# Optimization experiments

Hardware: AMD Instinct MI355X
Metric: run time of the kernel (lower is better)

Reference implementation:

```python
import jax, jax.numpy as jnp
import numpy as np

MIN_NORM = 1e-15
BALL_EPS = 1e-5  # keep points strictly inside the unit ball (c = 1)


def _artanh(x):
    return jnp.arctanh(jnp.clip(x, -1.0 + BALL_EPS, 1.0 - BALL_EPS))


def expmap0(u):
    # Poincare ball exp map at the origin, c = 1
    n = jnp.clip(jnp.linalg.norm(u, axis=-1, keepdims=True), MIN_NORM)
    return jnp.tanh(n) * u / n


def mobius_matvec(M, x):
    # Mobius matrix-vector product applied to every row of x: [N, D] -> [N, D]
    x_n = jnp.clip(jnp.linalg.norm(x, axis=-1, keepdims=True), MIN_NORM)
    Mx = x @ M.T
    Mx_n = jnp.clip(jnp.linalg.norm(Mx, axis=-1, keepdims=True), MIN_NORM)
    return jnp.tanh(Mx_n / x_n * _artanh(x_n)) * Mx / Mx_n


def pairwise_sqdist(x):
    # sqdist(x_i, x_j) for all pairs via mobius_add(-x_i, x_j); x: [N, D] -> [N, N]
    u = -x[:, None, :]          # [N, 1, D]
    v = x[None, :, :]           # [1, N, D]
    xy = jnp.sum(u * v, axis=-1, keepdims=True)   # [N, N, 1]
    x2 = jnp.sum(u * u, axis=-1, keepdims=True)
    y2 = jnp.sum(v * v, axis=-1, keepdims=True)
    num = (1.0 + 2.0 * xy + y2) * u + (1.0 - x2) * v   # [N, N, D]
    den = jnp.clip(1.0 + 2.0 * xy + x2 * y2, MIN_NORM)
    ma_n = jnp.linalg.norm(num / den, axis=-1)          # [N, N]
    d = 2.0 * _artanh(ma_n)
    return d * d


def setup_inputs() -> dict:
    key = jax.random.key(0)
    k1, k2, k3 = jax.random.split(key, 3)
    N, D, L = 512, 256, 2
    H_euc = jax.random.normal(k1, (N, D), dtype=jnp.float32)
    att_W = jax.random.normal(k2, (L, D, D), dtype=jnp.float32) / np.sqrt(D)
    A = jax.random.randint(k3, (N, N), 0, 2).astype(bool)
    return {"H_euc": H_euc, "att_W": att_W, "A": A}


def reference(H_euc, att_W, A):
    H = expmap0(H_euc)                      # [N, D] on the Poincare ball
    L = att_W.shape[0]
    for l in range(L):
        Wh = mobius_matvec(att_W[l], H)     # one mobius matvec per node (hoisted out of the i,j loop)
        scores = pairwise_sqdist(Wh)        # [N, N] hyperbolic squared distances
        scores = jnp.where(A, scores, -10000.0)
        att = jax.nn.softmax(scores, axis=1)
        att = jnp.where(A, att, 0.0)
        H = att @ H                         # [N, D]
    return H
```

## Files before the change

### kernel.cpp

```cpp
#include <hip/hip_runtime.h>
#include <math.h>

#define NN 512
#define DD 256

__device__ __forceinline__ void wred_sum2(double& a, double& b){
  #pragma unroll
  for (int o = 32; o > 0; o >>= 1){
    a += __shfl_down(a, o);
    b += __shfl_down(b, o);
  }
}
__device__ void bred_sum2(double& a, double& b){
  __shared__ double sa[4], sb[4]; __shared__ double ra, rb;
  int lane = threadIdx.x & 63, w = threadIdx.x >> 6;
  wred_sum2(a, b);
  __syncthreads();
  if (lane == 0){ sa[w] = a; sb[w] = b; }
  __syncthreads();
  if (threadIdx.x == 0){
    ra = (sa[0] + sa[1]) + (sa[2] + sa[3]);
    rb = (sb[0] + sb[1]) + (sb[2] + sb[3]);
  }
  __syncthreads();
  a = ra; b = rb;
}

__device__ __forceinline__ double artanh_clip(double x){
  const double lim = 1.0 - 1e-5;
  if (x >  lim) x =  lim;
  if (x < -lim) x = -lim;
  return 0.5 * log((1.0 + x) / (1.0 - x));
}

template<int MODE>
__global__ __launch_bounds__(256) void matvec_k(
    const float* __restrict__ Hin, const float* __restrict__ W,
    const double* __restrict__ hn2, float* __restrict__ Hf,
    float* __restrict__ Wh, float* __restrict__ WhT, double* __restrict__ r2){
  int b = blockIdx.x, t = threadIdx.x;
  int i0 = 2 * b, i1 = i0 + 1;
  __shared__ float h0s[DD], h1s[DD];
  float h0, h1;
  double xn0, xn1;
  if (MODE == 0){
    float u0 = Hin[i0 * DD + t], u1 = Hin[i1 * DD + t];
    double n0 = (double)u0 * (double)u0, n1 = (double)u1 * (double)u1;
    bred_sum2(n0, n1);
    n0 = sqrt(n0); if (n0 < 1e-15) n0 = 1e-15;
    n1 = sqrt(n1); if (n1 < 1e-15) n1 = 1e-15;
    double t0 = tanh(n0), t1 = tanh(n1);
    h0 = (float)(t0 / n0 * (double)u0);
    h1 = (float)(t1 / n1 * (double)u1);
    Hf[i0 * DD + t] = h0; Hf[i1 * DD + t] = h1;
    xn0 = t0; xn1 = t1;
    if (xn0 < 1e-15) xn0 = 1e-15;
    if (xn1 < 1e-15) xn1 = 1e-15;
  } else {
    h0 = Hin[i0 * DD + t]; h1 = Hin[i1 * DD + t];
    xn0 = sqrt(hn2[i0]); if (xn0 < 1e-15) xn0 = 1e-15;
    xn1 = sqrt(hn2[i1]); if (xn1 < 1e-15) xn1 = 1e-15;
  }
  h0s[t] = h0; h1s[t] = h1;
  __syncthreads();
  const float4* Wt = (const float4*)(W + t * DD);
  const float4* r0 = (const float4*)h0s;
  const float4* r1 = (const float4*)h1s;
  float4 A0 = {0,0,0,0}, A1 = {0,0,0,0};
  #pragma unroll 8
  for (int k = 0; k < DD / 4; k++){
    float4 w = Wt[k], x0 = r0[k], x1 = r1[k];
    A0.x = fmaf(x0.x, w.x, A0.x); A0.y = fmaf(x0.y, w.y, A0.y);
    A0.z = fmaf(x0.z, w.z, A0.z); A0.w = fmaf(x0.w, w.w, A0.w);
    A1.x = fmaf(x1.x, w.x, A1.x); A1.y = fmaf(x1.y, w.y, A1.y);
    A1.z = fmaf(x1.z, w.z, A1.z); A1.w = fmaf(x1.w, w.w, A1.w);
  }
  float mx0 = (A0.x + A0.y) + (A0.z + A0.w);
  float mx1 = (A1.x + A1.y) + (A1.z + A1.w);
  double m0 = (double)mx0 * (double)mx0, m1 = (double)mx1 * (double)mx1;
  bred_sum2(m0, m1);
  double mn0 = sqrt(m0); if (mn0 < 1e-15) mn0 = 1e-15;
  double mn1 = sqrt(m1); if (mn1 < 1e-15) mn1 = 1e-15;
  double th0 = tanh(mn0 / xn0 * artanh_clip(xn0));
  double th1 = tanh(mn1 / xn1 * artanh_clip(xn1));
  float w0 = (float)(mx0 * (th0 / mn0));
  float w1 = (float)(mx1 * (th1 / mn1));
  Wh[i0 * DD + t] = w0;  Wh[i1 * DD + t] = w1;
  WhT[t * NN + i0] = w0; WhT[t * NN + i1] = w1;
  if (t == 0){ r2[i0] = th0 * th0; r2[i1] = th1 * th1; }
}

__global__ __launch_bounds__(512) void fused_k(
    const float* __restrict__ Wh, const float* __restrict__ WhT,
    const double* __restrict__ r2, const int* __restrict__ A,
    const float* __restrict__ H, float* __restrict__ Hn, double* __restrict__ hn2){
  int b = blockIdx.x, tid = threadIdx.x;
  int i0 = 2 * b;
  __shared__ float xs[2 * DD];
  __shared__ float a_s[2][NN];
  __shared__ float4 parts[4 * 128 * 2];
  __shared__ double ssum[8];

  xs[tid] = Wh[i0 * DD + tid];
  __syncthreads();

  {
    int ks = tid >> 7, jq = tid & 127;
    const float4* WT4 = (const float4*)WhT;
    const float* x0 = xs, * x1 = xs + DD;
    float4 p0 = {0,0,0,0}, p1 = {0,0,0,0};
    int k0 = ks * 64;
    #pragma unroll 8
    for (int kk = 0; kk < 64; kk++){
      int k = k0 + kk;
      float4 w = WT4[k * 128 + jq];
      float a0v = x0[k], a1v = x1[k];
      p0.x = fmaf(a0v, w.x, p0.x); p0.y = fmaf(a0v, w.y, p0.y);
      p0.z = fmaf(a0v, w.z, p0.z); p0.w = fmaf(a0v, w.w, p0.w);
      p1.x = fmaf(a1v, w.x, p1.x); p1.y = fmaf(a1v, w.y, p1.y);
      p1.z = fmaf(a1v, w.z, p1.z); p1.w = fmaf(a1v, w.w, p1.w);
    }
    parts[(ks * 128 + jq) * 2 + 0] = p0;
    parts[(ks * 128 + jq) * 2 + 1] = p1;
  }
  __syncthreads();

  int r = tid >> 8, j2 = tid & 255;
  int i = i0 + r;
  double X2 = r2[i];
  const float* pf = (const float*)parts;

  auto dsum = [&](int j) -> double {
    int base = (((j >> 2) * 2 + r) << 2) + (j & 3);
    return ((double)pf[base] + (double)pf[base + 1024])
         + ((double)pf[base + 2048] + (double)pf[base + 3072]);
  };
  double d0 = dsum(j2), d1 = dsum(j2 + 256);

  auto score = [&](double dot, double Y2, int jj) -> double {
    if (i == jj) return 0.0;
    double xy = -dot;
    double a  = 1.0 + 2.0 * xy + Y2;
    double bb = 1.0 - X2;
    double den = 1.0 + 2.0 * xy + X2 * Y2;
    if (den < 1e-15) den = 1e-15;
    double nn = a * a * X2 + 2.0 * a * bb * xy + bb * bb * Y2;
    if (nn < 0.0) nn = 0.0;
    double s = sqrt(nn);
    double smax = den * (1.0 - 1e-5);
    if (s > smax) s = smax;
    double d = log((den + s) / (den - s));
    return d * d;
  };

  double Y0 = r2[j2], Y1 = r2[j2 + 256];
  int m0 = A[i * NN + j2], m1 = A[i * NN + j2 + 256];
  double e0 = 0.0, e1 = 0.0;
  if (m0) e0 = exp(score(d0, Y0, j2) - 150.0);
  if (m1) e1 = exp(score(d1, Y1, j2 + 256) - 150.0);

  double part = e0 + e1;
  #pragma unroll
  for (int o = 32; o > 0; o >>= 1) part += __shfl_down(part, o);
  int w = tid >> 6, lane = tid & 63;
  if (lane == 0) ssum[w] = part;
  __syncthreads();
  int base4 = r * 4;
  double sum = (ssum[base4] + ssum[base4 + 1]) + (ssum[base4 + 2] + ssum[base4 + 3]);
  double inv = 1.0 / sum;
  a_s[r][j2]       = m0 ? (float)(e0 * inv) : 0.f;
  a_s[r][j2 + 256] = m1 ? (float)(e1 * inv) : 0.f;
  __syncthreads();

  {
    int sg = tid >> 6, q = tid & 63;
    const float4* H4 = (const float4*)H;
    float4 c0 = {0,0,0,0}, c1 = {0,0,0,0};
    int jb = sg * 64;
    #pragma unroll 8
    for (int jj = 0; jj < 64; jj++){
      int j = jb + jj;
      float a0 = a_s[0][j], a1 = a_s[1][j];
      float4 h = H4[j * 64 + q];
      c0.x = fmaf(a0, h.x, c0.x); c0.y = fmaf(a0, h.y, c0.y);
      c0.z = fmaf(a0, h.z, c0.z); c0.w = fmaf(a0, h.w, c0.w);
      c1.x = fmaf(a1, h.x, c1.x); c1.y = fmaf(a1, h.y, c1.y);
      c1.z = fmaf(a1, h.z, c1.z); c1.w = fmaf(a1, h.w, c1.w);
    }
    float4* part2 = parts;
    part2[sg * 64 + q]       = c0;
    part2[512 + sg * 64 + q] = c1;
  }
  __syncthreads();
  if (tid < 128){
    int rr = tid >> 6, qq = tid & 63;
    const float4* part2 = parts;
    float4 p[8];
    #pragma unroll
    for (int s8 = 0; s8 < 8; s8++) p[s8] = part2[rr * 512 + s8 * 64 + qq];
    float4 o;
    o.x = ((p[0].x + p[1].x) + (p[2].x + p[3].x)) + ((p[4].x + p[5].x) + (p[6].x + p[7].x));
    o.y = ((p[0].y + p[1].y) + (p[2].y + p[3].y)) + ((p[4].y + p[5].y) + (p[6].y + p[7].y));
    o.z = ((p[0].z + p[1].z) + (p[2].z + p[3].z)) + ((p[4].z + p[5].z) + (p[6].z + p[7].z));
    o.w = ((p[0].w + p[1].w) + (p[2].w + p[3].w)) + ((p[4].w + p[5].w) + (p[6].w + p[7].w));
    ((float4*)(Hn + (i0 + rr) * DD))[qq] = o;
    double s = (double)o.x * o.x + (double)o.y * o.y
             + (double)o.z * o.z + (double)o.w * o.w;
    #pragma unroll
    for (int off = 32; off > 0; off >>= 1) s += __shfl_down(s, off);
    if (qq == 0) hn2[i0 + rr] = s;
  }
}

extern "C" void kernel_launch(void* const* d_in, const int* in_sizes, int n_in,
                              void* d_out, int out_size, void* d_ws, size_t ws_size,
                              hipStream_t stream){
  const float* H_euc = (const float*)d_in[0];
  const float* W     = (const float*)d_in[1];
  const int*   A     = (const int*)d_in[2];
  float* out = (float*)d_out;

  float* Hf  = (float*)d_ws;
  float* Hn  = Hf + NN * DD;
  float* Wh  = Hn + NN * DD;
  float* WhT = Wh + NN * DD;
  double* r2  = (double*)(WhT + NN * DD);
  double* hn2 = r2 + NN;

  matvec_k<0><<<NN / 2, DD, 0, stream>>>(H_euc, W, nullptr, Hf, Wh, WhT, r2);
  fused_k    <<<NN / 2, 2 * DD, 0, stream>>>(Wh, WhT, r2, A, Hf, Hn, hn2);
  matvec_k<1><<<NN / 2, DD, 0, stream>>>(Hn, W + DD * DD, hn2, nullptr, Wh, WhT, r2);
  fused_k    <<<NN / 2, 2 * DD, 0, stream>>>(Wh, WhT, r2, A, Hn, out, hn2);
}
```

Measured before the change: 61.14 us.

## Fuse layer-2 mobius matvec into layer-1 attention kernel and prefetch H rows

The second layer's mobius matvec now runs at the tail of the first fused attention kernel, since each block already holds the two new H rows it produced. The second weight matrix is transposed once by the first 16 blocks of the initial matvec kernel, which removes one launch and a global round trip of Hn. The fused kernel also loads 8 H rows into registers before the softmax phase and widens the x loads in the distance GEMV to float4. The cost is more shared memory and registers per block, and the extra work lengthens the first fused kernel.

```diff
diff --git a/kernel.cpp b/kernel.cpp
--- a/kernel.cpp
+++ b/kernel.cpp
@@ -33,34 +33,26 @@
   return 0.5 * log((1.0 + x) / (1.0 - x));
 }
 
-template<int MODE>
-__global__ __launch_bounds__(256) void matvec_k(
+__global__ __launch_bounds__(256) void matvec0_k(
     const float* __restrict__ Hin, const float* __restrict__ W,
-    const double* __restrict__ hn2, float* __restrict__ Hf,
-    float* __restrict__ Wh, float* __restrict__ WhT, double* __restrict__ r2){
+    const float* __restrict__ W1, float* __restrict__ W1T,
+    float* __restrict__ Hf, float* __restrict__ Wh, float* __restrict__ WhT,
+    double* __restrict__ r2){
+  __shared__ float h0s[DD], h1s[DD];
+  __shared__ float tile[64][65];
   int b = blockIdx.x, t = threadIdx.x;
   int i0 = 2 * b, i1 = i0 + 1;
-  __shared__ float h0s[DD], h1s[DD];
-  float h0, h1;
-  double xn0, xn1;
-  if (MODE == 0){
-    float u0 = Hin[i0 * DD + t], u1 = Hin[i1 * DD + t];
-    double n0 = (double)u0 * (double)u0, n1 = (double)u1 * (double)u1;
-    bred_sum2(n0, n1);
-    n0 = sqrt(n0); if (n0 < 1e-15) n0 = 1e-15;
-    n1 = sqrt(n1); if (n1 < 1e-15) n1 = 1e-15;
-    double t0 = tanh(n0), t1 = tanh(n1);
-    h0 = (float)(t0 / n0 * (double)u0);
-    h1 = (float)(t1 / n1 * (double)u1);
-    Hf[i0 * DD + t] = h0; Hf[i1 * DD + t] = h1;
-    xn0 = t0; xn1 = t1;
-    if (xn0 < 1e-15) xn0 = 1e-15;
-    if (xn1 < 1e-15) xn1 = 1e-15;
-  } else {
-    h0 = Hin[i0 * DD + t]; h1 = Hin[i1 * DD + t];
-    xn0 = sqrt(hn2[i0]); if (xn0 < 1e-15) xn0 = 1e-15;
-    xn1 = sqrt(hn2[i1]); if (xn1 < 1e-15) xn1 = 1e-15;
-  }
+  float u0 = Hin[i0 * DD + t], u1 = Hin[i1 * DD + t];
+  double n0 = (double)u0 * (double)u0, n1 = (double)u1 * (double)u1;
+  bred_sum2(n0, n1);
+  n0 = sqrt(n0); if (n0 < 1e-15) n0 = 1e-15;
+  n1 = sqrt(n1); if (n1 < 1e-15) n1 = 1e-15;
+  double t0 = tanh(n0), t1 = tanh(n1);
+  float h0 = (float)(t0 / n0 * (double)u0);
+  float h1 = (float)(t1 / n1 * (double)u1);
+  Hf[i0 * DD + t] = h0; Hf[i1 * DD + t] = h1;
+  double xn0 = t0 < 1e-15 ? 1e-15 : t0;
+  double xn1 = t1 < 1e-15 ? 1e-15 : t1;
   h0s[t] = h0; h1s[t] = h1;
   __syncthreads();
   const float4* Wt = (const float4*)(W + t * DD);
@@ -88,18 +80,35 @@
   Wh[i0 * DD + t] = w0;  Wh[i1 * DD + t] = w1;
   WhT[t * NN + i0] = w0; WhT[t * NN + i1] = w1;
   if (t == 0){ r2[i0] = th0 * th0; r2[i1] = th1 * th1; }
-}
-
+
+  if (b < 16){
+    int tr = b >> 2, tc = b & 3;
+    int tx = t & 63, ty4 = t >> 6;
+    #pragma unroll
+    for (int yy = 0; yy < 64; yy += 4)
+      tile[yy + ty4][tx] = W1[(tr * 64 + yy + ty4) * DD + tc * 64 + tx];
+    __syncthreads();
+    #pragma unroll
+    for (int yy = 0; yy < 64; yy += 4)
+      W1T[(tc * 64 + yy + ty4) * DD + tr * 64 + tx] = tile[tx][yy + ty4];
+  }
+}
+
+template<bool LAST>
 __global__ __launch_bounds__(512) void fused_k(
     const float* __restrict__ Wh, const float* __restrict__ WhT,
     const double* __restrict__ r2, const int* __restrict__ A,
-    const float* __restrict__ H, float* __restrict__ Hn, double* __restrict__ hn2){
+    const float* __restrict__ H, const float* __restrict__ WT2,
+    float* __restrict__ Hn, float* __restrict__ Whn,
+    float* __restrict__ WhTn, double* __restrict__ r2n){
   int b = blockIdx.x, tid = threadIdx.x;
   int i0 = 2 * b;
   __shared__ float xs[2 * DD];
   __shared__ float a_s[2][NN];
-  __shared__ float4 parts[4 * 128 * 2];
+  __shared__ float4 parts[1024];
   __shared__ double ssum[8];
+  __shared__ float hn_s[2][DD];
+  __shared__ double hnorm2[2];
 
   xs[tid] = Wh[i0 * DD + tid];
   __syncthreads();
@@ -107,29 +116,47 @@
   {
     int ks = tid >> 7, jq = tid & 127;
     const float4* WT4 = (const float4*)WhT;
-    const float* x0 = xs, * x1 = xs + DD;
+    const float4* x04 = (const float4*)xs;
+    const float4* x14 = (const float4*)(xs + DD);
     float4 p0 = {0,0,0,0}, p1 = {0,0,0,0};
-    int k0 = ks * 64;
-    #pragma unroll 8
-    for (int kk = 0; kk < 64; kk++){
-      int k = k0 + kk;
-      float4 w = WT4[k * 128 + jq];
-      float a0v = x0[k], a1v = x1[k];
-      p0.x = fmaf(a0v, w.x, p0.x); p0.y = fmaf(a0v, w.y, p0.y);
-      p0.z = fmaf(a0v, w.z, p0.z); p0.w = fmaf(a0v, w.w, p0.w);
-      p1.x = fmaf(a1v, w.x, p1.x); p1.y = fmaf(a1v, w.y, p1.y);
-      p1.z = fmaf(a1v, w.z, p1.z); p1.w = fmaf(a1v, w.w, p1.w);
+    int kq0 = ks * 16;
+    #pragma unroll 4
+    for (int kk = 0; kk < 16; kk++){
+      float4 xa = x04[kq0 + kk], xb = x14[kq0 + kk];
+      const float4* wp = WT4 + (kq0 + kk) * 4 * 128 + jq;
+      float4 w0 = wp[0], w1 = wp[128], w2 = wp[256], w3 = wp[384];
+      p0.x = fmaf(xa.x, w0.x, p0.x); p0.y = fmaf(xa.x, w0.y, p0.y);
+      p0.z = fmaf(xa.x, w0.z, p0.z); p0.w = fmaf(xa.x, w0.w, p0.w);
+      p0.x = fmaf(xa.y, w1.x, p0.x); p0.y = fmaf(xa.y, w1.y, p0.y);
+      p0.z = fmaf(xa.y, w1.z, p0.z); p0.w = fmaf(xa.y, w1.w, p0.w);
+      p0.x = fmaf(xa.z, w2.x, p0.x); p0.y = fmaf(xa.z, w2.y, p0.y);
+      p0.z = fmaf(xa.z, w2.z, p0.z); p0.w = fmaf(xa.z, w2.w, p0.w);
+      p0.x = fmaf(xa.w, w3.x, p0.x); p0.y = fmaf(xa.w, w3.y, p0.y);
+      p0.z = fmaf(xa.w, w3.z, p0.z); p0.w = fmaf(xa.w, w3.w, p0.w);
+      p1.x = fmaf(xb.x, w0.x, p1.x); p1.y = fmaf(xb.x, w0.y, p1.y);
+      p1.z = fmaf(xb.x, w0.z, p1.z); p1.w = fmaf(xb.x, w0.w, p1.w);
+      p1.x = fmaf(xb.y, w1.x, p1.x); p1.y = fmaf(xb.y, w1.y, p1.y);
+      p1.z = fmaf(xb.y, w1.z, p1.z); p1.w = fmaf(xb.y, w1.w, p1.w);
+      p1.x = fmaf(xb.z, w2.x, p1.x); p1.y = fmaf(xb.z, w2.y, p1.y);
+      p1.z = fmaf(xb.z, w2.z, p1.z); p1.w = fmaf(xb.z, w2.w, p1.w);
+      p1.x = fmaf(xb.w, w3.x, p1.x); p1.y = fmaf(xb.w, w3.y, p1.y);
+      p1.z = fmaf(xb.w, w3.z, p1.z); p1.w = fmaf(xb.w, w3.w, p1.w);
     }
     parts[(ks * 128 + jq) * 2 + 0] = p0;
     parts[(ks * 128 + jq) * 2 + 1] = p1;
   }
   __syncthreads();
+
+  int sgC = tid >> 6, qC = tid & 63;
+  const float4* H4 = (const float4*)H;
+  float4 hpre[8];
+  #pragma unroll
+  for (int jj = 0; jj < 8; jj++) hpre[jj] = H4[(sgC * 64 + jj) * 64 + qC];
 
   int r = tid >> 8, j2 = tid & 255;
   int i = i0 + r;
   double X2 = r2[i];
   const float* pf = (const float*)parts;
-
   auto dsum = [&](int j) -> double {
     int base = (((j >> 2) * 2 + r) << 2) + (j & 3);
     return ((double)pf[base] + (double)pf[base + 1024])
@@ -173,42 +200,100 @@
   __syncthreads();
 
   {
-    int sg = tid >> 6, q = tid & 63;
-    const float4* H4 = (const float4*)H;
     float4 c0 = {0,0,0,0}, c1 = {0,0,0,0};
-    int jb = sg * 64;
-    #pragma unroll 8
-    for (int jj = 0; jj < 64; jj++){
+    int jb = sgC * 64;
+    #pragma unroll
+    for (int jj = 0; jj < 8; jj++){
       int j = jb + jj;
       float a0 = a_s[0][j], a1 = a_s[1][j];
-      float4 h = H4[j * 64 + q];
+      float4 h = hpre[jj];
       c0.x = fmaf(a0, h.x, c0.x); c0.y = fmaf(a0, h.y, c0.y);
       c0.z = fmaf(a0, h.z, c0.z); c0.w = fmaf(a0, h.w, c0.w);
       c1.x = fmaf(a1, h.x, c1.x); c1.y = fmaf(a1, h.y, c1.y);
       c1.z = fmaf(a1, h.z, c1.z); c1.w = fmaf(a1, h.w, c1.w);
     }
-    float4* part2 = parts;
-    part2[sg * 64 + q]       = c0;
-    part2[512 + sg * 64 + q] = c1;
+    #pragma unroll 8
+    for (int jj = 8; jj < 64; jj++){
+      int j = jb + jj;
+      float a0 = a_s[0][j], a1 = a_s[1][j];
+      float4 h = H4[j * 64 + qC];
+      c0.x = fmaf(a0, h.x, c0.x); c0.y = fmaf(a0, h.y, c0.y);
+      c0.z = fmaf(a0, h.z, c0.z); c0.w = fmaf(a0, h.w, c0.w);
+      c1.x = fmaf(a1, h.x, c1.x); c1.y = fmaf(a1, h.y, c1.y);
+      c1.z = fmaf(a1, h.z, c1.z); c1.w = fmaf(a1, h.w, c1.w);
+    }
+    parts[sgC * 64 + qC]       = c0;
+    parts[512 + sgC * 64 + qC] = c1;
   }
   __syncthreads();
   if (tid < 128){
     int rr = tid >> 6, qq = tid & 63;
-    const float4* part2 = parts;
     float4 p[8];
     #pragma unroll
-    for (int s8 = 0; s8 < 8; s8++) p[s8] = part2[rr * 512 + s8 * 64 + qq];
+    for (int s8 = 0; s8 < 8; s8++) p[s8] = parts[rr * 512 + s8 * 64 + qq];
     float4 o;
     o.x = ((p[0].x + p[1].x) + (p[2].x + p[3].x)) + ((p[4].x + p[5].x) + (p[6].x + p[7].x));
     o.y = ((p[0].y + p[1].y) + (p[2].y + p[3].y)) + ((p[4].y + p[5].y) + (p[6].y + p[7].y));
     o.z = ((p[0].z + p[1].z) + (p[2].z + p[3].z)) + ((p[4].z + p[5].z) + (p[6].z + p[7].z));
     o.w = ((p[0].w + p[1].w) + (p[2].w + p[3].w)) + ((p[4].w + p[5].w) + (p[6].w + p[7].w));
     ((float4*)(Hn + (i0 + rr) * DD))[qq] = o;
-    double s = (double)o.x * o.x + (double)o.y * o.y
-             + (double)o.z * o.z + (double)o.w * o.w;
-    #pragma unroll
-    for (int off = 32; off > 0; off >>= 1) s += __shfl_down(s, off);
-    if (qq == 0) hn2[i0 + rr] = s;
+    if (!LAST){
+      ((float4*)hn_s[rr])[qq] = o;
+      double s = (double)o.x * o.x + (double)o.y * o.y
+               + (double)o.z * o.z + (double)o.w * o.w;
+      #pragma unroll
+      for (int off = 32; off > 0; off >>= 1) s += __shfl_down(s, off);
+      if (qq == 0) hnorm2[rr] = s;
+    }
+  }
+  if (LAST) return;
+  __syncthreads();
+
+  {
+    int ks2 = tid >> 6, dq = tid & 63;
+    const float4* WT4b = (const float4*)WT2;
+    const float* h0 = hn_s[0]; const float* h1 = hn_s[1];
+    float4 p0 = {0,0,0,0}, p1 = {0,0,0,0};
+    int k0 = ks2 * 32;
+    #pragma unroll 8
+    for (int kk = 0; kk < 32; kk++){
+      int k = k0 + kk;
+      float4 wv = WT4b[k * 64 + dq];
+      float a0v = h0[k], a1v = h1[k];
+      p0.x = fmaf(a0v, wv.x, p0.x); p0.y = fmaf(a0v, wv.y, p0.y);
+      p0.z = fmaf(a0v, wv.z, p0.z); p0.w = fmaf(a0v, wv.w, p0.w);
+      p1.x = fmaf(a1v, wv.x, p1.x); p1.y = fmaf(a1v, wv.y, p1.y);
+      p1.z = fmaf(a1v, wv.z, p1.z); p1.w = fmaf(a1v, wv.w, p1.w);
+    }
+    parts[(ks2 * 64 + dq) * 2 + 0] = p0;
+    parts[(ks2 * 64 + dq) * 2 + 1] = p1;
+  }
+  __syncthreads();
+  {
+    int rr = tid >> 8, d = tid & 255;
+    const float* pf2 = (const float*)parts;
+    int base = ((d >> 2) * 2 + rr) * 4 + (d & 3);
+    float q0 = pf2[base]        + pf2[base + 512];
+    float q1 = pf2[base + 1024] + pf2[base + 1536];
+    float q2 = pf2[base + 2048] + pf2[base + 2560];
+    float q3 = pf2[base + 3072] + pf2[base + 3584];
+    float mx = (q0 + q1) + (q2 + q3);
+    double m2 = (double)mx * (double)mx;
+    #pragma unroll
+    for (int o = 32; o > 0; o >>= 1) m2 += __shfl_down(m2, o);
+    int w2 = tid >> 6, lane2 = tid & 63;
+    if (lane2 == 0) ssum[w2] = m2;
+    __syncthreads();
+    int b4 = rr * 4;
+    double m2sum = (ssum[b4] + ssum[b4 + 1]) + (ssum[b4 + 2] + ssum[b4 + 3]);
+    double mn = sqrt(m2sum); if (mn < 1e-15) mn = 1e-15;
+    double xn = sqrt(hnorm2[rr]); if (xn < 1e-15) xn = 1e-15;
+    double th = tanh(mn / xn * artanh_clip(xn));
+    float wv = (float)((double)mx * (th / mn));
+    int irow = i0 + rr;
+    Whn[irow * DD + d] = wv;
+    WhTn[d * NN + irow] = wv;
+    if (d == 0) r2n[irow] = th * th;
   }
 }
 
@@ -220,15 +305,17 @@
   const int*   A     = (const int*)d_in[2];
   float* out = (float*)d_out;
 
-  float* Hf  = (float*)d_ws;
-  float* Hn  = Hf + NN * DD;
-  float* Wh  = Hn + NN * DD;
-  float* WhT = Wh + NN * DD;
-  double* r2  = (double*)(WhT + NN * DD);
-  double* hn2 = r2 + NN;
-
-  matvec_k<0><<<NN / 2, DD, 0, stream>>>(H_euc, W, nullptr, Hf, Wh, WhT, r2);
-  fused_k    <<<NN / 2, 2 * DD, 0, stream>>>(Wh, WhT, r2, A, Hf, Hn, hn2);
-  matvec_k<1><<<NN / 2, DD, 0, stream>>>(Hn, W + DD * DD, hn2, nullptr, Wh, WhT, r2);
-  fused_k    <<<NN / 2, 2 * DD, 0, stream>>>(Wh, WhT, r2, A, Hn, out, hn2);
-}
+  float* Hf   = (float*)d_ws;
+  float* Hn   = Hf   + NN * DD;
+  float* Wh   = Hn   + NN * DD;
+  float* WhT  = Wh   + NN * DD;
+  float* Whb  = WhT  + NN * DD;
+  float* WhTb = Whb  + NN * DD;
+  float* W1T  = WhTb + NN * DD;
+  double* r2  = (double*)(W1T + DD * DD);
+  double* r2b = r2 + NN;
+
+  matvec0_k<<<NN / 2, DD, 0, stream>>>(H_euc, W, W + DD * DD, W1T, Hf, Wh, WhT, r2);
+  fused_k<false><<<NN / 2, 2 * DD, 0, stream>>>(Wh, WhT, r2, A, Hf, W1T, Hn, Whb, WhTb, r2b);
+  fused_k<true> <<<NN / 2, 2 * DD, 0, stream>>>(Whb, WhTb, r2b, A, Hn, nullptr, out, nullptr, nullptr, nullptr);
+}
```

After: 52.92 us. -13.4%, faster.
